# Kernel optimization log

Hardware: AMD Instinct MI355X
Metric: run time of the kernel (lower is better)

## Reference

```python
import jax, jax.numpy as jnp
import numpy as np
from jax import lax

M = 4096
B = 1024
NSTEPS = 199   # loop runs 200 iters; backward+Adam.step happen on iters 1..199
LR = 0.1
B1, B2, EPS = 0.9, 0.999, 1e-8  # torch.optim.Adam defaults


def setup_inputs() -> dict:
    key = jax.random.key(0)
    k1, k2, k3 = jax.random.split(key, 3)
    mean = jax.random.normal(k1, (M,), dtype=jnp.float32)
    va = jax.random.normal(k2, (M, M), dtype=jnp.float32)
    xt = jax.random.normal(k3, (B, 1, M), dtype=jnp.float32)
    return {"mean": mean, "va": va, "xt": xt}


def reference(mean, va, xt):
    # Loss: f(w) = 0.5*(w-m)^T Q (w-m) + sum_i log(1 + exp(-x_i @ m))
    # The second (logistic) term uses m, not w -> constant gradient-wise.
    # grad_w f = 0.5*(Q + Q^T)(w - m). 199 Adam steps, lr=0.1, w0 = ones.
    m_col = mean[:, None]                      # (M, 1)
    Qs = 0.5 * (va + va.T)                     # symmetrized, precomputed once
    w0 = jnp.ones((M, 1), dtype=mean.dtype)
    zeros = jnp.zeros_like(w0)

    def adam_step(carry, t):
        w, mt, vt = carry
        g = Qs @ (w - m_col)                   # (M, 1) matvec
        mt = B1 * mt + (1.0 - B1) * g
        vt = B2 * vt + (1.0 - B2) * g * g
        bc1 = 1.0 - jnp.power(jnp.float32(B1), t)
        bc2 = 1.0 - jnp.power(jnp.float32(B2), t)
        denom = jnp.sqrt(vt) / jnp.sqrt(bc2) + EPS  # torch Adam formulation
        w = w - (LR / bc1) * mt / denom
        return (w, mt, vt), None

    ts = jnp.arange(1, NSTEPS + 1, dtype=jnp.float32)
    (w, _, _), _ = lax.scan(adam_step, (w0, zeros, zeros), ts)
    return w[:, 0]                             # squeeze -> (M,)
```

## Files before the change

### kernel.cpp

```cpp
#include <hip/hip_runtime.h>
#include <math.h>

#define MDIM   4096
#define NSTEPS 199
#define NBLK   256
#define NTHR   1024
#define B1C    0.9f
#define B2C    0.999f
#define EPSC   1e-8f

__global__ void prep_qs(const float* __restrict__ va, float* __restrict__ Qs) {
    __shared__ float tile[32][33];
    const int j0 = blockIdx.x * 32;
    const int i0 = blockIdx.y * 32;
    const int tx = threadIdx.x, ty = threadIdx.y;

    for (int k = 0; k < 32; k += 8)
        tile[ty + k][tx] = va[(size_t)(j0 + ty + k) * MDIM + i0 + tx];
    __syncthreads();
    for (int k = 0; k < 32; k += 8) {
        int i = i0 + ty + k;
        float a = va[(size_t)i * MDIM + j0 + tx];
        float b = tile[tx][ty + k];
        Qs[(size_t)i * MDIM + j0 + tx] = 0.5f * (a + b);
    }
}

__global__ void init_state(const float* __restrict__ mean,
                           float* __restrict__ u0,
                           int* __restrict__ flags, int nflags) {
    int i = blockIdx.x * blockDim.x + threadIdx.x;
    if (i < MDIM)   u0[i] = 1.0f - mean[i];
    if (i < nflags) flags[i] = 0;
}

__global__ __launch_bounds__(NTHR) void adam_persist(
        const float* __restrict__ Qs,
        float* u0, float* u1,
        const float* __restrict__ mean,
        float* __restrict__ w_out,
        int* __restrict__ flags) {
    __shared__ float su[MDIM];
    float4* su4 = (float4*)su;

    const int tid  = threadIdx.x;
    const int bid  = blockIdx.x;
    const int wave = tid >> 6;
    const int lane = tid & 63;
    const int row  = bid * 16 + wave;

    float4 qreg[16];
    const float4* qrow4 = (const float4*)(Qs + (size_t)row * MDIM);
#pragma unroll
    for (int it = 0; it < 16; ++it) qreg[it] = qrow4[lane + 64 * it];

    float m = 0.0f, v = 0.0f, b1p = 1.0f, b2p = 1.0f, unew = 0.0f;

    for (int t = 1; t <= NSTEPS; ++t) {
        const float* uin  = (t & 1) ? u0 : u1;
        float*       uout = (t & 1) ? u1 : u0;

#pragma unroll
        for (int k = 0; k < 4; ++k) {
            int idx = tid + NTHR * k;
            su[idx] = __hip_atomic_load(uin + idx, __ATOMIC_RELAXED,
                                        __HIP_MEMORY_SCOPE_AGENT);
        }
        __syncthreads();

        float acc = 0.0f;
#pragma unroll
        for (int it = 0; it < 16; ++it) {
            float4 q = qreg[it];
            float4 u = su4[lane + 64 * it];
            acc += q.x * u.x + q.y * u.y + q.z * u.z + q.w * u.w;
        }
#pragma unroll
        for (int off = 32; off > 0; off >>= 1) acc += __shfl_xor(acc, off);
        const float g = acc;

        b1p *= B1C;
        b2p *= B2C;
        m = B1C * m + (1.0f - B1C) * g;
        v = B2C * v + (1.0f - B2C) * g * g;
        const float denom = sqrtf(v) / sqrtf(1.0f - b2p) + EPSC;
        unew = su[row] - (0.1f / (1.0f - b1p)) * m / denom;

        if (lane == 0)
            __hip_atomic_store(uout + row, unew, __ATOMIC_RELAXED,
                               __HIP_MEMORY_SCOPE_AGENT);
        __syncthreads();

        if (tid == 0)
            __hip_atomic_store(flags + t * NBLK + bid, 1, __ATOMIC_RELAXED,
                               __HIP_MEMORY_SCOPE_AGENT);

        if (tid < 64) {
            const int* f = flags + t * NBLK + 4 * tid;
            int spin = 0;
            for (;;) {
                int s0 = __hip_atomic_load(f + 0, __ATOMIC_RELAXED, __HIP_MEMORY_SCOPE_AGENT);
                int s1 = __hip_atomic_load(f + 1, __ATOMIC_RELAXED, __HIP_MEMORY_SCOPE_AGENT);
                int s2 = __hip_atomic_load(f + 2, __ATOMIC_RELAXED, __HIP_MEMORY_SCOPE_AGENT);
                int s3 = __hip_atomic_load(f + 3, __ATOMIC_RELAXED, __HIP_MEMORY_SCOPE_AGENT);
                if ((s0 & s1 & s2 & s3) != 0) break;
                if (++spin > (1 << 25)) break;
            }
        }
        __syncthreads();
    }

    if (lane == 0) w_out[row] = unew + mean[row];
}

extern "C" void kernel_launch(void* const* d_in, const int* in_sizes, int n_in,
                              void* d_out, int out_size, void* d_ws, size_t ws_size,
                              hipStream_t stream) {
    const float* mean = (const float*)d_in[0];
    const float* va   = (const float*)d_in[1];
    float* w_out = (float*)d_out;

    float* ws = (float*)d_ws;
    float* Qs  = ws;
    float* u0  = ws + (size_t)MDIM * MDIM;
    float* u1  = u0 + MDIM;
    int*   flg = (int*)(u1 + MDIM);

    const int nflags = (NSTEPS + 1) * NBLK;

    prep_qs<<<dim3(MDIM / 32, MDIM / 32), dim3(32, 8), 0, stream>>>(va, Qs);
    init_state<<<(nflags + 255) / 256, 256, 0, stream>>>(mean, u0, flg, nflags);

    void* args[] = { (void*)&Qs, (void*)&u0, (void*)&u1,
                     (void*)&mean, (void*)&w_out, (void*)&flg };
    hipLaunchCooperativeKernel((const void*)adam_persist,
                               dim3(NBLK), dim3(NTHR), args, 0, stream);
}
```

Before: 1.144 ms.

## Replace flag grid barrier with step-tagged packed values and double-buffered LDS

Each shared vector element is now stored as a 64-bit word holding the float value and the step number that wrote it. Readers spin on the vector itself until every element carries the expected step tag, which replaces the separate flag array, the per-step grid barrier and one of the block-level barriers. The LDS copy of the vector is double-buffered by step parity, so the barrier at the end of each step can be dropped. In exchange, global vector traffic doubles, and every block now polls the whole 32 KB vector instead of a small flag array, which may add L2 contention while it waits.

```diff
diff --git a/kernel.cpp b/kernel.cpp
--- a/kernel.cpp
+++ b/kernel.cpp
@@ -8,6 +8,14 @@
 #define B1C    0.9f
 #define B2C    0.999f
 #define EPSC   1e-8f
+
+typedef unsigned long long u64;
+
+__device__ __forceinline__ u64 pack_uv(float v, unsigned t) {
+    return ((u64)t << 32) | (u64)__float_as_uint(v);
+}
+__device__ __forceinline__ float    unpack_v(u64 p) { return __uint_as_float((unsigned)p); }
+__device__ __forceinline__ unsigned unpack_t(u64 p) { return (unsigned)(p >> 32); }
 
 __global__ void prep_qs(const float* __restrict__ va, float* __restrict__ Qs) {
     __shared__ float tile[32][33];
@@ -26,22 +34,17 @@
     }
 }
 
-__global__ void init_state(const float* __restrict__ mean,
-                           float* __restrict__ u0,
-                           int* __restrict__ flags, int nflags) {
+__global__ void init_state(const float* __restrict__ mean, u64* __restrict__ u0) {
     int i = blockIdx.x * blockDim.x + threadIdx.x;
-    if (i < MDIM)   u0[i] = 1.0f - mean[i];
-    if (i < nflags) flags[i] = 0;
+    if (i < MDIM) u0[i] = pack_uv(1.0f - mean[i], 0u);
 }
 
 __global__ __launch_bounds__(NTHR) void adam_persist(
         const float* __restrict__ Qs,
-        float* u0, float* u1,
+        u64* u0, u64* u1,
         const float* __restrict__ mean,
-        float* __restrict__ w_out,
-        int* __restrict__ flags) {
-    __shared__ float su[MDIM];
-    float4* su4 = (float4*)su;
+        float* __restrict__ w_out) {
+    __shared__ float su[2][MDIM];
 
     const int tid  = threadIdx.x;
     const int bid  = blockIdx.x;
@@ -56,23 +59,40 @@
 
     float m = 0.0f, v = 0.0f, b1p = 1.0f, b2p = 1.0f, unew = 0.0f;
 
+    const int i0 = tid;
+    const int i1 = tid + NTHR;
+    const int i2 = tid + 2 * NTHR;
+    const int i3 = tid + 3 * NTHR;
+
     for (int t = 1; t <= NSTEPS; ++t) {
-        const float* uin  = (t & 1) ? u0 : u1;
-        float*       uout = (t & 1) ? u1 : u0;
+        u64* uin  = (t & 1) ? u0 : u1;
+        u64* uout = (t & 1) ? u1 : u0;
+        const unsigned tg = (unsigned)(t - 1);
+        const int b = t & 1;
 
-#pragma unroll
-        for (int k = 0; k < 4; ++k) {
-            int idx = tid + NTHR * k;
-            su[idx] = __hip_atomic_load(uin + idx, __ATOMIC_RELAXED,
-                                        __HIP_MEMORY_SCOPE_AGENT);
+        u64 q0, q1, q2, q3;
+        int spin = 0;
+        for (;;) {
+            q0 = __hip_atomic_load(uin + i0, __ATOMIC_RELAXED, __HIP_MEMORY_SCOPE_AGENT);
+            q1 = __hip_atomic_load(uin + i1, __ATOMIC_RELAXED, __HIP_MEMORY_SCOPE_AGENT);
+            q2 = __hip_atomic_load(uin + i2, __ATOMIC_RELAXED, __HIP_MEMORY_SCOPE_AGENT);
+            q3 = __hip_atomic_load(uin + i3, __ATOMIC_RELAXED, __HIP_MEMORY_SCOPE_AGENT);
+            if ((unpack_t(q0) == tg) & (unpack_t(q1) == tg) &
+                (unpack_t(q2) == tg) & (unpack_t(q3) == tg)) break;
+            if (++spin > (1 << 18)) break;
         }
+        su[b][i0] = unpack_v(q0);
+        su[b][i1] = unpack_v(q1);
+        su[b][i2] = unpack_v(q2);
+        su[b][i3] = unpack_v(q3);
         __syncthreads();
 
         float acc = 0.0f;
+        const float4* sbuf4 = (const float4*)su[b];
 #pragma unroll
         for (int it = 0; it < 16; ++it) {
             float4 q = qreg[it];
-            float4 u = su4[lane + 64 * it];
+            float4 u = sbuf4[lane + 64 * it];
             acc += q.x * u.x + q.y * u.y + q.z * u.z + q.w * u.w;
         }
 #pragma unroll
@@ -84,30 +104,11 @@
         m = B1C * m + (1.0f - B1C) * g;
         v = B2C * v + (1.0f - B2C) * g * g;
         const float denom = sqrtf(v) / sqrtf(1.0f - b2p) + EPSC;
-        unew = su[row] - (0.1f / (1.0f - b1p)) * m / denom;
+        unew = su[b][row] - (0.1f / (1.0f - b1p)) * m / denom;
 
         if (lane == 0)
-            __hip_atomic_store(uout + row, unew, __ATOMIC_RELAXED,
-                               __HIP_MEMORY_SCOPE_AGENT);
-        __syncthreads();
-
-        if (tid == 0)
-            __hip_atomic_store(flags + t * NBLK + bid, 1, __ATOMIC_RELAXED,
-                               __HIP_MEMORY_SCOPE_AGENT);
-
-        if (tid < 64) {
-            const int* f = flags + t * NBLK + 4 * tid;
-            int spin = 0;
-            for (;;) {
-                int s0 = __hip_atomic_load(f + 0, __ATOMIC_RELAXED, __HIP_MEMORY_SCOPE_AGENT);
-                int s1 = __hip_atomic_load(f + 1, __ATOMIC_RELAXED, __HIP_MEMORY_SCOPE_AGENT);
-                int s2 = __hip_atomic_load(f + 2, __ATOMIC_RELAXED, __HIP_MEMORY_SCOPE_AGENT);
-                int s3 = __hip_atomic_load(f + 3, __ATOMIC_RELAXED, __HIP_MEMORY_SCOPE_AGENT);
-                if ((s0 & s1 & s2 & s3) != 0) break;
-                if (++spin > (1 << 25)) break;
-            }
-        }
-        __syncthreads();
+            __hip_atomic_store(uout + row, pack_uv(unew, (unsigned)t),
+                               __ATOMIC_RELAXED, __HIP_MEMORY_SCOPE_AGENT);
     }
 
     if (lane == 0) w_out[row] = unew + mean[row];
@@ -121,18 +122,15 @@
     float* w_out = (float*)d_out;
 
     float* ws = (float*)d_ws;
-    float* Qs  = ws;
-    float* u0  = ws + (size_t)MDIM * MDIM;
-    float* u1  = u0 + MDIM;
-    int*   flg = (int*)(u1 + MDIM);
-
-    const int nflags = (NSTEPS + 1) * NBLK;
+    float* Qs = ws;
+    u64*   u0 = (u64*)(ws + (size_t)MDIM * MDIM);
+    u64*   u1 = u0 + MDIM;
 
     prep_qs<<<dim3(MDIM / 32, MDIM / 32), dim3(32, 8), 0, stream>>>(va, Qs);
-    init_state<<<(nflags + 255) / 256, 256, 0, stream>>>(mean, u0, flg, nflags);
+    init_state<<<(MDIM + 255) / 256, 256, 0, stream>>>(mean, u0);
 
     void* args[] = { (void*)&Qs, (void*)&u0, (void*)&u1,
-                     (void*)&mean, (void*)&w_out, (void*)&flg };
+                     (void*)&mean, (void*)&w_out };
     hipLaunchCooperativeKernel((const void*)adam_persist,
                                dim3(NBLK), dim3(NTHR), args, 0, stream);
 }
```

After: 1.670 ms. +46.0%, slower.
